# Kernel tuning notes

Measured on AMD Instinct MI355X. Metric: run time of the kernel, lower is better.

## Reference

```python
import jax, jax.numpy as jnp
import numpy as np

N_NODES = 500_000
N_FEAT = 125          # embedding dim; cat with pos(3) -> 128
HIDDEN = 128
OUT_DIM = 64
N_TYPES = 100
N_GRAPHS = 4096


def setup_inputs() -> dict:
    key = jax.random.key(0)
    ks = jax.random.split(key, 10)
    pos = jax.random.normal(ks[0], (N_NODES, 3), dtype=jnp.float32)
    z = jax.random.randint(ks[1], (N_NODES,), 0, N_TYPES)
    batch = jnp.sort(jax.random.randint(ks[2], (N_NODES,), 0, N_GRAPHS))
    emb = jax.random.normal(ks[3], (N_TYPES, N_FEAT), dtype=jnp.float32)
    s1 = 1.0 / np.sqrt(N_FEAT + 3)
    s2 = 1.0 / np.sqrt(HIDDEN)
    W1 = jax.random.normal(ks[4], (N_FEAT + 3, HIDDEN), dtype=jnp.float32) * s1
    b1 = jnp.zeros((HIDDEN,), dtype=jnp.float32)
    W2 = jax.random.normal(ks[5], (HIDDEN, HIDDEN), dtype=jnp.float32) * s2
    b2 = jnp.zeros((HIDDEN,), dtype=jnp.float32)
    W3 = jax.random.normal(ks[6], (HIDDEN, OUT_DIM), dtype=jnp.float32) * s2
    b3 = jnp.zeros((OUT_DIM,), dtype=jnp.float32)
    return {"pos": pos, "z": z, "batch": batch, "emb": emb,
            "W1": W1, "b1": b1, "W2": W2, "b2": b2, "W3": W3, "b3": b3}


def reference(pos, z, batch, emb, W1, b1, W2, b2, W3, b3):
    # embed node types and concat with 3D positions  -> [N, 128]
    x = jnp.concatenate([pos, emb[z]], axis=-1)
    # two equivariant-transformer layers (per-node transform) + relu
    x = jax.nn.relu(x @ W1 + b1)   # [N, H]
    x = jax.nn.relu(x @ W2 + b2)   # [N, H]
    # output head
    x = x @ W3 + b3                # [N, O]
    # global mean pool per graph
    s = jax.ops.segment_sum(x, batch, num_segments=N_GRAPHS)                    # [G, O]
    cnt = jax.ops.segment_sum(jnp.ones((x.shape[0], 1), x.dtype), batch,
                              num_segments=N_GRAPHS)                            # [G, 1]
    return s / jnp.maximum(cnt, 1.0)
```

## Files before the change

### kernel.cpp

```cpp
#include <hip/hip_runtime.h>
#include <hip/hip_bf16.h>

#define N_NODES 500000
#define N_FEAT 125
#define HID 128
#define OUTD 64
#define N_GRAPHS 4096
#define N_TYPES 100
#define WTILE 32
#define NTILES32 (N_NODES / WTILE)
#define NBLOCKS 256
#define NWAVES 8
#define WPAD 136
#define OPADF 68

typedef float f32x4 __attribute__((ext_vector_type(4)));
typedef short s16x8 __attribute__((ext_vector_type(8)));

#define OFF_T 0
#define SZ_T (N_TYPES * WPAD * 2)
#define OFF_W2 (OFF_T + SZ_T)
#define OFF_W3 (OFF_W2 + HID * WPAD * 2)
#define OFF_B2 (OFF_W3 + OUTD * WPAD * 2)
#define OFF_SCR (OFF_B2 + HID * 4)
#define SCR_BYTES (WTILE * WPAD * 2)
#define OFF_IDS (OFF_SCR + NWAVES * SCR_BYTES)
#define LDS_BYTES (OFF_IDS + NWAVES * WTILE * 4)

#define WS_GSUM 0
#define WS_GCNT ((size_t)N_GRAPHS * OUTD * 4)
#define WS_T    (WS_GCNT + (size_t)N_GRAPHS * 4)
#define WS_ZERO WS_T

__device__ __forceinline__ unsigned short f2bf(float f) {
  union { float f; unsigned u; } v; v.f = f;
  unsigned r = v.u + 0x7FFFu + ((v.u >> 16) & 1u);
  return (unsigned short)(r >> 16);
}
__device__ __forceinline__ float bf2f(unsigned short u) {
  union { unsigned u; float f; } v; v.u = ((unsigned)u) << 16;
  return v.f;
}
__device__ __forceinline__ unsigned pk2bf(float a, float b) {
  __hip_bfloat162 h = __float22bfloat162_rn(float2{a, b});
  union { __hip_bfloat162 h; unsigned u; } v; v.h = h;
  return v.u;
}

__device__ __forceinline__ void wavefence() {
  __builtin_amdgcn_sched_barrier(0);
  __builtin_amdgcn_wave_barrier();
  __builtin_amdgcn_sched_barrier(0);
}

extern "C" __global__ void gnn_prep(const float* __restrict__ emb,
                                    const float* __restrict__ W1,
                                    const float* __restrict__ b1,
                                    unsigned short* __restrict__ Tg)
{
  const int g = blockIdx.x, j = threadIdx.x;
  float acc = b1[j];
  const float* er = emb + g * N_FEAT;
  for (int k = 0; k < N_FEAT; ++k)
    acc = fmaf(er[k], W1[(3 + k) * HID + j], acc);
  Tg[g * HID + j] = f2bf(acc);
}

extern "C" __global__ void __launch_bounds__(512, 2)
gnn_main(const float* __restrict__ pos, const int* __restrict__ z,
         const int* __restrict__ batch, const unsigned short* __restrict__ Tg,
         const float* __restrict__ W1, const float* __restrict__ W2,
         const float* __restrict__ b2, const float* __restrict__ W3,
         float* __restrict__ gsum, int* __restrict__ gcnt)
{
  extern __shared__ char lds[];
  unsigned short* Tl  = (unsigned short*)(lds + OFF_T);
  unsigned short* w2t = (unsigned short*)(lds + OFF_W2);
  unsigned short* w3t = (unsigned short*)(lds + OFF_W3);
  float* bias2 = (float*)(lds + OFF_B2);

  const int t = threadIdx.x;

  for (int i = t; i < N_TYPES * HID; i += 512) {
    int g = i >> 7, f = i & 127;
    Tl[g * WPAD + f] = Tg[i];
  }
  for (int i = t; i < HID * HID; i += 512) {
    int k = i >> 7, n = i & 127;
    w2t[n * WPAD + k] = f2bf(W2[i]);
  }
  for (int i = t; i < HID * OUTD; i += 512) {
    int k = i >> 6, n = i & 63;
    w3t[n * WPAD + k] = f2bf(W3[i]);
  }
  if (t < HID) bias2[t] = b2[t];

  const int wave = t >> 6, lane = t & 63, quad = lane >> 4, l15 = lane & 15;
  unsigned short* xs = (unsigned short*)(lds + OFF_SCR + wave * SCR_BYTES);
  float* xo = (float*)xs;
  int* ids = (int*)(lds + OFF_IDS) + wave * WTILE;

  float w1r[3][4][8];
  #pragma unroll
  for (int c = 0; c < 3; ++c)
    #pragma unroll
    for (int k = 0; k < 4; ++k)
      #pragma unroll
      for (int j = 0; j < 8; ++j)
        w1r[c][k][j] = W1[c * HID + k * 32 + quad * 8 + j];

  __syncthreads();

  const int gwave = blockIdx.x * NWAVES + wave;

  for (int tile = gwave; tile < NTILES32; tile += NBLOCKS * NWAVES) {
    const int base = tile * WTILE;

    if (lane < WTILE) ids[lane] = batch[base + lane];

    s16x8 a[2][4];
    #pragma unroll
    for (int m = 0; m < 2; ++m) {
      const int node = base + m * 16 + l15;
      const int zi = z[node];
      const float px = pos[node * 3], py = pos[node * 3 + 1], pz = pos[node * 3 + 2];
      const unsigned short* Tr = Tl + zi * WPAD;
      #pragma unroll
      for (int k = 0; k < 4; ++k) {
        s16x8 tf = *(const s16x8*)(Tr + k * 32 + quad * 8);
        s16x8 fr;
        #pragma unroll
        for (int j = 0; j < 8; j += 2) {
          float v0 = bf2f((unsigned short)tf[j])
                   + px * w1r[0][k][j] + py * w1r[1][k][j] + pz * w1r[2][k][j];
          float v1 = bf2f((unsigned short)tf[j + 1])
                   + px * w1r[0][k][j + 1] + py * w1r[1][k][j + 1] + pz * w1r[2][k][j + 1];
          ((unsigned*)&fr)[j >> 1] = pk2bf(fmaxf(v0, 0.f), fmaxf(v1, 0.f));
        }
        a[m][k] = fr;
      }
    }

    f32x4 acc[8][2] = {};
    #pragma unroll
    for (int oi = 0; oi < 8; ++oi)
      #pragma unroll
      for (int k = 0; k < 4; ++k) {
        s16x8 w = *(const s16x8*)(w2t + (oi * 16 + l15) * WPAD + k * 32 + quad * 8);
        acc[oi][0] = __builtin_amdgcn_mfma_f32_16x16x32_bf16(w, a[0][k], acc[oi][0], 0, 0, 0);
        acc[oi][1] = __builtin_amdgcn_mfma_f32_16x16x32_bf16(w, a[1][k], acc[oi][1], 0, 0, 0);
      }
    #pragma unroll
    for (int oi = 0; oi < 8; ++oi) {
      const int f0 = oi * 16 + quad * 4;
      f32x4 bv = *(const f32x4*)(bias2 + f0);
      #pragma unroll
      for (int m = 0; m < 2; ++m) {
        unsigned lo = pk2bf(fmaxf(acc[oi][m][0] + bv[0], 0.f),
                            fmaxf(acc[oi][m][1] + bv[1], 0.f));
        unsigned hi = pk2bf(fmaxf(acc[oi][m][2] + bv[2], 0.f),
                            fmaxf(acc[oi][m][3] + bv[3], 0.f));
        *(uint2*)(xs + (m * 16 + l15) * WPAD + f0) = uint2{lo, hi};
      }
    }
    wavefence();
    #pragma unroll
    for (int m = 0; m < 2; ++m)
      #pragma unroll
      for (int k = 0; k < 4; ++k)
        a[m][k] = *(const s16x8*)(xs + (m * 16 + l15) * WPAD + k * 32 + quad * 8);
    wavefence();

    f32x4 acc3[4][2] = {};
    #pragma unroll
    for (int oi = 0; oi < 4; ++oi)
      #pragma unroll
      for (int k = 0; k < 4; ++k) {
        s16x8 w = *(const s16x8*)(w3t + (oi * 16 + l15) * WPAD + k * 32 + quad * 8);
        acc3[oi][0] = __builtin_amdgcn_mfma_f32_16x16x32_bf16(w, a[0][k], acc3[oi][0], 0, 0, 0);
        acc3[oi][1] = __builtin_amdgcn_mfma_f32_16x16x32_bf16(w, a[1][k], acc3[oi][1], 0, 0, 0);
      }
    #pragma unroll
    for (int oi = 0; oi < 4; ++oi)
      #pragma unroll
      for (int m = 0; m < 2; ++m)
        *(f32x4*)(xo + (m * 16 + l15) * OPADF + oi * 16 + quad * 4) = acc3[oi][m];
    wavefence();

    {
      const int o = lane;
      int cur = ids[0];
      float run = 0.f; int rc = 0;
      #pragma unroll 1
      for (int n = 0; n < WTILE; ++n) {
        int bb = ids[n];
        if (bb != cur) {
          atomicAdd(&gsum[cur * OUTD + o], run);
          if (o == 0) atomicAdd(&gcnt[cur], rc);
          run = 0.f; rc = 0; cur = bb;
        }
        run += xo[n * OPADF + o]; rc++;
      }
      atomicAdd(&gsum[cur * OUTD + o], run);
      if (o == 0) atomicAdd(&gcnt[cur], rc);
    }
    wavefence();
  }
}

extern "C" __global__ void gnn_finalize(const float* __restrict__ gsum,
                                        const int* __restrict__ gcnt,
                                        const float* __restrict__ b3,
                                        float* __restrict__ out)
{
  int i = blockIdx.x * 256 + threadIdx.x;
  if (i < N_GRAPHS * OUTD) {
    int g = i >> 6, o = i & 63;
    int c = gcnt[g];
    out[i] = (c > 0) ? (gsum[i] / (float)c + b3[o]) : 0.f;
  }
}

extern "C" void kernel_launch(void* const* d_in, const int* in_sizes, int n_in,
                              void* d_out, int out_size, void* d_ws, size_t ws_size,
                              hipStream_t stream) {
  const float* pos  = (const float*)d_in[0];
  const int*   z    = (const int*)d_in[1];
  const int*   batch= (const int*)d_in[2];
  const float* emb  = (const float*)d_in[3];
  const float* W1   = (const float*)d_in[4];
  const float* b1   = (const float*)d_in[5];
  const float* W2   = (const float*)d_in[6];
  const float* b2   = (const float*)d_in[7];
  const float* W3   = (const float*)d_in[8];
  const float* b3   = (const float*)d_in[9];

  float* gsum = (float*)d_ws;
  int*   gcnt = (int*)((char*)d_ws + WS_GCNT);
  unsigned short* Tg = (unsigned short*)((char*)d_ws + WS_T);

  hipMemsetAsync(d_ws, 0, WS_ZERO, stream);

  hipLaunchKernelGGL(gnn_prep, dim3(N_TYPES), dim3(HID), 0, stream, emb, W1, b1, Tg);

  hipFuncSetAttribute((const void*)gnn_main,
                      hipFuncAttributeMaxDynamicSharedMemorySize, LDS_BYTES);
  hipLaunchKernelGGL(gnn_main, dim3(NBLOCKS), dim3(512), LDS_BYTES, stream,
                     pos, z, batch, Tg, W1, W2, b2, W3, gsum, gcnt);
  hipLaunchKernelGGL(gnn_finalize, dim3((N_GRAPHS * OUTD + 255) / 256), dim3(256), 0, stream,
                     gsum, gcnt, b3, (float*)d_out);
}
```

Measured before the change: 148.2 us.

## Fuse memset, prep, main and finalize into one cooperative kernel with grid syncs

Replaces the memset, the prep kernel, the main kernel and the finalize kernel with a single cooperative launch. Zeroing and the embedding-table precompute run first across the grid, a grid sync follows, each block copies the packed table into LDS, and a second grid sync precedes the in-kernel mean-pool finalize. This removes three extra launches and the gaps between them. In exchange it adds two grid-wide barriers and requires all 256 blocks to be co-resident for the cooperative launch.

```diff
diff --git a/kernel.cpp b/kernel.cpp
--- a/kernel.cpp
+++ b/kernel.cpp
@@ -1,5 +1,8 @@
 #include <hip/hip_runtime.h>
 #include <hip/hip_bf16.h>
+#include <hip/hip_cooperative_groups.h>
+
+namespace cg = cooperative_groups;
 
 #define N_NODES 500000
 #define N_FEAT 125
@@ -10,7 +13,9 @@
 #define WTILE 32
 #define NTILES32 (N_NODES / WTILE)
 #define NBLOCKS 256
+#define NTHREADS 512
 #define NWAVES 8
+#define GRID_THREADS (NBLOCKS * NTHREADS)
 #define WPAD 136
 #define OPADF 68
 
@@ -29,8 +34,9 @@
 
 #define WS_GSUM 0
 #define WS_GCNT ((size_t)N_GRAPHS * OUTD * 4)
-#define WS_T    (WS_GCNT + (size_t)N_GRAPHS * 4)
-#define WS_ZERO WS_T
+#define WS_TPK  (WS_GCNT + (size_t)N_GRAPHS * 4)
+#define ZERO_DWORDS ((N_GRAPHS * OUTD + N_GRAPHS))
+#define N_TPK (N_TYPES * (HID / 2))
 
 __device__ __forceinline__ unsigned short f2bf(float f) {
   union { float f; unsigned u; } v; v.f = f;
@@ -53,25 +59,14 @@
   __builtin_amdgcn_sched_barrier(0);
 }
 
-extern "C" __global__ void gnn_prep(const float* __restrict__ emb,
-                                    const float* __restrict__ W1,
-                                    const float* __restrict__ b1,
-                                    unsigned short* __restrict__ Tg)
-{
-  const int g = blockIdx.x, j = threadIdx.x;
-  float acc = b1[j];
-  const float* er = emb + g * N_FEAT;
-  for (int k = 0; k < N_FEAT; ++k)
-    acc = fmaf(er[k], W1[(3 + k) * HID + j], acc);
-  Tg[g * HID + j] = f2bf(acc);
-}
-
-extern "C" __global__ void __launch_bounds__(512, 2)
-gnn_main(const float* __restrict__ pos, const int* __restrict__ z,
-         const int* __restrict__ batch, const unsigned short* __restrict__ Tg,
-         const float* __restrict__ W1, const float* __restrict__ W2,
-         const float* __restrict__ b2, const float* __restrict__ W3,
-         float* __restrict__ gsum, int* __restrict__ gcnt)
+extern "C" __global__ void __launch_bounds__(NTHREADS, 2)
+gnn_fused(const float* __restrict__ pos, const int* __restrict__ z,
+          const int* __restrict__ batch, const float* __restrict__ emb,
+          const float* __restrict__ W1, const float* __restrict__ b1,
+          const float* __restrict__ W2, const float* __restrict__ b2,
+          const float* __restrict__ W3, const float* __restrict__ b3,
+          float* __restrict__ gsum, int* __restrict__ gcnt,
+          unsigned* __restrict__ Tpk, float* __restrict__ out)
 {
   extern __shared__ char lds[];
   unsigned short* Tl  = (unsigned short*)(lds + OFF_T);
@@ -80,20 +75,45 @@
   float* bias2 = (float*)(lds + OFF_B2);
 
   const int t = threadIdx.x;
-
-  for (int i = t; i < N_TYPES * HID; i += 512) {
-    int g = i >> 7, f = i & 127;
-    Tl[g * WPAD + f] = Tg[i];
-  }
-  for (int i = t; i < HID * HID; i += 512) {
+  const int gid = blockIdx.x * NTHREADS + t;
+
+  {
+    unsigned* wz = (unsigned*)gsum;
+    for (int i = gid; i < ZERO_DWORDS; i += GRID_THREADS)
+      __hip_atomic_store(&wz[i], 0u, __ATOMIC_RELAXED, __HIP_MEMORY_SCOPE_AGENT);
+
+    if (gid < N_TPK) {
+      const int g = gid >> 6, jp = gid & 63, j0 = 2 * jp;
+      const float* er = emb + g * N_FEAT;
+      float2 b = *(const float2*)&b1[j0];
+      float a0 = b.x, a1 = b.y;
+      for (int k = 0; k < N_FEAT; ++k) {
+        float e = er[k];
+        float2 w = *(const float2*)&W1[(3 + k) * HID + j0];
+        a0 = fmaf(e, w.x, a0); a1 = fmaf(e, w.y, a1);
+      }
+      __hip_atomic_store(&Tpk[gid], pk2bf(a0, a1),
+                         __ATOMIC_RELAXED, __HIP_MEMORY_SCOPE_AGENT);
+    }
+  }
+
+  for (int i = t; i < HID * HID; i += NTHREADS) {
     int k = i >> 7, n = i & 127;
     w2t[n * WPAD + k] = f2bf(W2[i]);
   }
-  for (int i = t; i < HID * OUTD; i += 512) {
+  for (int i = t; i < HID * OUTD; i += NTHREADS) {
     int k = i >> 6, n = i & 63;
     w3t[n * WPAD + k] = f2bf(W3[i]);
   }
   if (t < HID) bias2[t] = b2[t];
+
+  cg::this_grid().sync();
+
+  for (int i = t; i < N_TPK; i += NTHREADS) {
+    unsigned u = __hip_atomic_load(&Tpk[i], __ATOMIC_RELAXED, __HIP_MEMORY_SCOPE_AGENT);
+    int g = i >> 6, jp = i & 63;
+    *(unsigned*)(Tl + g * WPAD + 2 * jp) = u;
+  }
 
   const int wave = t >> 6, lane = t & 63, quad = lane >> 4, l15 = lane & 15;
   unsigned short* xs = (unsigned short*)(lds + OFF_SCR + wave * SCR_BYTES);
@@ -206,18 +226,17 @@
     }
     wavefence();
   }
-}
-
-extern "C" __global__ void gnn_finalize(const float* __restrict__ gsum,
-                                        const int* __restrict__ gcnt,
-                                        const float* __restrict__ b3,
-                                        float* __restrict__ out)
-{
-  int i = blockIdx.x * 256 + threadIdx.x;
-  if (i < N_GRAPHS * OUTD) {
+
+  __threadfence();
+  cg::this_grid().sync();
+
+  #pragma unroll
+  for (int rep = 0; rep < (N_GRAPHS * OUTD) / GRID_THREADS; ++rep) {
+    int i = gid + rep * GRID_THREADS;
     int g = i >> 6, o = i & 63;
-    int c = gcnt[g];
-    out[i] = (c > 0) ? (gsum[i] / (float)c + b3[o]) : 0.f;
+    int c = __hip_atomic_load(&gcnt[g], __ATOMIC_RELAXED, __HIP_MEMORY_SCOPE_AGENT);
+    float s = __hip_atomic_load(&gsum[i], __ATOMIC_RELAXED, __HIP_MEMORY_SCOPE_AGENT);
+    out[i] = (c > 0) ? (s / (float)c + b3[o]) : 0.f;
   }
 }
 
@@ -235,18 +254,16 @@
   const float* W3   = (const float*)d_in[8];
   const float* b3   = (const float*)d_in[9];
 
-  float* gsum = (float*)d_ws;
-  int*   gcnt = (int*)((char*)d_ws + WS_GCNT);
-  unsigned short* Tg = (unsigned short*)((char*)d_ws + WS_T);
-
-  hipMemsetAsync(d_ws, 0, WS_ZERO, stream);
-
-  hipLaunchKernelGGL(gnn_prep, dim3(N_TYPES), dim3(HID), 0, stream, emb, W1, b1, Tg);
-
-  hipFuncSetAttribute((const void*)gnn_main,
+  float*    gsum = (float*)d_ws;
+  int*      gcnt = (int*)((char*)d_ws + WS_GCNT);
+  unsigned* Tpk  = (unsigned*)((char*)d_ws + WS_TPK);
+  float*    outp = (float*)d_out;
+
+  hipFuncSetAttribute((const void*)gnn_fused,
                       hipFuncAttributeMaxDynamicSharedMemorySize, LDS_BYTES);
-  hipLaunchKernelGGL(gnn_main, dim3(NBLOCKS), dim3(512), LDS_BYTES, stream,
-                     pos, z, batch, Tg, W1, W2, b2, W3, gsum, gcnt);
-  hipLaunchKernelGGL(gnn_finalize, dim3((N_GRAPHS * OUTD + 255) / 256), dim3(256), 0, stream,
-                     gsum, gcnt, b3, (float*)d_out);
-}
+
+  void* args[] = {&pos, &z, &batch, &emb, &W1, &b1, &W2, &b2, &W3, &b3,
+                  &gsum, &gcnt, &Tpk, &outp};
+  hipLaunchCooperativeKernel((void*)gnn_fused, dim3(NBLOCKS), dim3(NTHREADS),
+                             args, LDS_BYTES, stream);
+}
```

Result: slower. 242.2 us (+63.4%).
